# Performance work log

Hardware: AMD Instinct MI355X
Metric: run time of the kernel (lower is better)

The kernel has to match this reference:

```python
import jax, jax.numpy as jnp
import numpy as np

NUM_HEADS = 8
NUM_GROUPS = 8
EPS = 1e-5


def group_norm(x, gamma, beta):
    # x: [B, C, H, W], 8 groups over channel dim
    B, C, H, W = x.shape
    xg = x.reshape(B, NUM_GROUPS, C // NUM_GROUPS, H, W)
    mean = xg.mean(axis=(2, 3, 4), keepdims=True)
    var = xg.var(axis=(2, 3, 4), keepdims=True)
    xn = ((xg - mean) * jax.lax.rsqrt(var + EPS)).reshape(B, C, H, W)
    return xn * gamma[None, :, None, None] + beta[None, :, None, None]


def conv1x1(x, w, b):
    # w: [O, C] (1x1 conv kernel squeezed), x: [B, C, H, W]
    return jnp.einsum('oc,bchw->bohw', w, x) + b[None, :, None, None]


def setup_inputs() -> dict:
    key = jax.random.key(0)
    ks = jax.random.split(key, 6)
    B, C, H, W = 16, 512, 32, 32
    x = jax.random.normal(ks[0], (B, C, H, W), dtype=jnp.float32)
    norm_w = jnp.ones((C,), jnp.float32)
    norm_b = jnp.zeros((C,), jnp.float32)
    s = 1.0 / np.sqrt(C)
    qkv_w = jax.random.uniform(ks[1], (3 * C, C), jnp.float32, -s, s)
    qkv_b = jax.random.uniform(ks[2], (3 * C,), jnp.float32, -s, s)
    proj_w = jax.random.uniform(ks[3], (C, C), jnp.float32, -s, s)
    proj_b = jax.random.uniform(ks[4], (C,), jnp.float32, -s, s)
    return {"x": x, "norm_w": norm_w, "norm_b": norm_b,
            "qkv_w": qkv_w, "qkv_b": qkv_b, "proj_w": proj_w, "proj_b": proj_b}


def reference(x, norm_w, norm_b, qkv_w, qkv_b, proj_w, proj_b):
    B, C, H, W = x.shape
    hd = C // NUM_HEADS  # head dim
    h = group_norm(x, norm_w, norm_b)
    qkv = conv1x1(h, qkv_w, qkv_b)                 # [B, 3C, H, W]
    q, k, v = jnp.split(qkv, 3, axis=1)
    q = q.reshape(B, NUM_HEADS, hd, H * W)
    k = k.reshape(B, NUM_HEADS, hd, H * W)
    v = v.reshape(B, NUM_HEADS, hd, H * W)
    scale = hd ** (-0.5)
    attn = jax.nn.softmax(jnp.einsum('bhci,bhcj->bhij', q, k) * scale, axis=-1)
    h = jnp.einsum('bhij,bhcj->bhci', attn, v).reshape(B, C, H, W)
    h = conv1x1(h, proj_w, proj_b)
    return x + h
```

## Files before the change

### kernel.cpp

```cpp
#include <hip/hip_runtime.h>
#include <hip/hip_bf16.h>


typedef __bf16 bf16;
typedef __attribute__((ext_vector_type(8))) __bf16 bf16x8;
typedef __attribute__((ext_vector_type(4))) float f32x4;
typedef __attribute__((ext_vector_type(16))) float f32x16;
typedef __attribute__((ext_vector_type(4))) unsigned int u32x4;

#define SCALE_Q 0.18033688f

__device__ __forceinline__ bf16x8 ld8(const bf16* p) {
    return *reinterpret_cast<const bf16x8*>(p);
}

__device__ __forceinline__ void gl_lds16(const void* g, void* l) {
    __builtin_amdgcn_global_load_lds(
        (const __attribute__((address_space(1))) void*)g,
        (__attribute__((address_space(3))) void*)l, 16, 0, 0);
}

__global__ __launch_bounds__(256) void cvt_weights(const float* __restrict__ qkv_w,
                                                   const float* __restrict__ proj_w,
                                                   bf16* __restrict__ dst) {
    const int N1 = 1536 * 512;
    int i = (blockIdx.x * 256 + threadIdx.x) * 4;
    float4 f = (i < N1) ? *reinterpret_cast<const float4*>(qkv_w + i)
                        : *reinterpret_cast<const float4*>(proj_w + (i - N1));
    dst[i + 0] = (bf16)f.x;
    dst[i + 1] = (bf16)f.y;
    dst[i + 2] = (bf16)f.z;
    dst[i + 3] = (bf16)f.w;
}

__global__ __launch_bounds__(256) void gn_fused(const float* __restrict__ x,
                                                const float* __restrict__ gamma,
                                                const float* __restrict__ beta,
                                                bf16* __restrict__ hnT) {
    int bg = blockIdx.x;
    int b = bg >> 3, g = bg & 7;
    const float* base = x + (size_t)bg * 65536;
    int t = threadIdx.x;
    int wave = t >> 6, lane = t & 63;

    float s = 0.f, sq = 0.f;
    for (int i = t * 4; i < 65536; i += 256 * 4) {
        float4 f = *reinterpret_cast<const float4*>(base + i);
        s += f.x + f.y + f.z + f.w;
        sq += f.x * f.x + f.y * f.y + f.z * f.z + f.w * f.w;
    }
    #pragma unroll
    for (int off = 32; off > 0; off >>= 1) {
        s += __shfl_down(s, off);
        sq += __shfl_down(sq, off);
    }
    __shared__ float ls[4], lq[4];
    __shared__ float2 st;
    if (lane == 0) { ls[wave] = s; lq[wave] = sq; }
    __syncthreads();
    if (t == 0) {
        s = ls[0] + ls[1] + ls[2] + ls[3];
        sq = lq[0] + lq[1] + lq[2] + lq[3];
        float mean = s * (1.f / 65536.f);
        float var = sq * (1.f / 65536.f) - mean * mean;
        st = make_float2(mean, rsqrtf(var + 1e-5f));
    }
    __syncthreads();
    float mean = st.x, rstd = st.y;

    __shared__ float tile[64][65];
    int cl = t & 63;
    float ga = gamma[g * 64 + cl] * rstd;
    float be = beta[g * 64 + cl] - mean * ga;
    for (int pt = 0; pt < 16; pt++) {
        const float* xb = base + pt * 64;
        #pragma unroll
        for (int r = 0; r < 16; r++) {
            int crow = r * 4 + (t >> 6);
            tile[crow][t & 63] = xb[(size_t)crow * 1024 + (t & 63)];
        }
        __syncthreads();
        bf16* ob = hnT + ((size_t)b * 1024 + pt * 64) * 512 + g * 64 + cl;
        #pragma unroll
        for (int r = 0; r < 16; r++) {
            int pl = r * 4 + (t >> 6);
            ob[(size_t)pl * 512] = (bf16)(tile[cl][pl] * ga + be);
        }
        __syncthreads();
    }
}

__device__ __forceinline__ void gemm_stage(const bf16* __restrict__ A,
                                           const bf16* __restrict__ B,
                                           char* smem, int buf,
                                           int m_blk, int n_blk, int k0,
                                           int wave, int lane) {
    char* Al = smem + buf * 32768;
    char* Bl = Al + 16384;
    #pragma unroll
    for (int i = 0; i < 4; i++) {
        int seg = i * 4 + wave;
        int r = seg * 8 + (lane >> 3);
        int cg = (lane & 7) ^ (r & 7);
        gl_lds16((const char*)(A + (size_t)(m_blk + r) * 512 + k0) + cg * 16,
                 Al + seg * 1024);
        gl_lds16((const char*)(B + (size_t)(n_blk + r) * 512 + k0) + cg * 16,
                 Bl + seg * 1024);
    }
}

__device__ __forceinline__ void gemm_compute(const char* smem, int buf,
                                             int wave, int lane,
                                             f32x4 (&acc)[4][4]) {
    const char* Al = smem + buf * 32768;
    const char* Bl = Al + 16384;
    int l15 = lane & 15, hi = lane >> 4;
    int mb = (wave >> 1) * 64, nb = (wave & 1) * 64;
    #pragma unroll
    for (int kc = 0; kc < 2; kc++) {
        int ck = kc * 4 + hi;
        bf16x8 a[4], b[4];
        #pragma unroll
        for (int mf = 0; mf < 4; mf++) {
            int row = mb + mf * 16 + l15;
            a[mf] = *reinterpret_cast<const bf16x8*>(Al + row * 128 + (ck ^ (row & 7)) * 16);
        }
        #pragma unroll
        for (int nf = 0; nf < 4; nf++) {
            int row = nb + nf * 16 + l15;
            b[nf] = *reinterpret_cast<const bf16x8*>(Bl + row * 128 + (ck ^ (row & 7)) * 16);
        }
        #pragma unroll
        for (int mf = 0; mf < 4; mf++)
            #pragma unroll
            for (int nf = 0; nf < 4; nf++)
                acc[mf][nf] = __builtin_amdgcn_mfma_f32_16x16x32_bf16(
                    a[mf], b[nf], acc[mf][nf], 0, 0, 0);
    }
}

#define GEMM_LDS_LOOP(A_, B_, SMEM_)                            \
    f32x4 acc[4][4] = {};                                       \
    {                                                           \
        gemm_stage(A_, B_, SMEM_, 0, m_blk, n_blk, 0, wave, lane); \
        __syncthreads();                                        \
        int buf = 0;                                            \
        for (int ks = 0; ks < 8; ks++) {                        \
            if (ks < 7)                                         \
                gemm_stage(A_, B_, SMEM_, buf ^ 1, m_blk, n_blk, (ks + 1) * 64, wave, lane); \
            gemm_compute(SMEM_, buf, wave, lane, acc);          \
            __syncthreads();                                    \
            buf ^= 1;                                           \
        }                                                       \
    }

__global__ __launch_bounds__(256, 2) void gemm_qkv(const bf16* __restrict__ hnT,
                                                   const bf16* __restrict__ wqkv,
                                                   const float* __restrict__ qkv_b,
                                                   bf16* __restrict__ qk_t,
                                                   bf16* __restrict__ vbuf) {
    __shared__ char smem[65536];
    int b = blockIdx.z;
    int wave = threadIdx.x >> 6, lane = threadIdx.x & 63;
    int l15 = lane & 15;
    int y = blockIdx.y;
    if (y < 8) {
        int m_blk = blockIdx.x * 128;
        int n_blk = y * 128;
        const bf16* A = hnT + (size_t)b * 1024 * 512;
        GEMM_LDS_LOOP(A, wqkv, smem)
        bf16* out = qk_t + (size_t)b * 1024 * 1024;
        int col0 = n_blk + (wave & 1) * 64 + l15;
        int row0 = m_blk + (wave >> 1) * 64 + (lane >> 4) * 4;
        #pragma unroll
        for (int nf = 0; nf < 4; nf++) {
            int col = col0 + nf * 16;
            float bias = qkv_b[col];
            float scl = (col < 512) ? SCALE_Q : 1.0f;
            #pragma unroll
            for (int mf = 0; mf < 4; mf++)
                #pragma unroll
                for (int r = 0; r < 4; r++)
                    out[(size_t)(row0 + mf * 16 + r) * 1024 + col] =
                        (bf16)((acc[mf][nf][r] + bias) * scl);
        }
    } else {
        int m_blk = (y - 8) * 128;
        int n_blk = blockIdx.x * 128;
        const bf16* A = wqkv + (size_t)1024 * 512;
        const bf16* Bm = hnT + (size_t)b * 1024 * 512;
        GEMM_LDS_LOOP(A, Bm, smem)
        bf16* out = vbuf + (size_t)b * 512 * 1024;
        int col0 = n_blk + (wave & 1) * 64 + l15;
        int row0 = m_blk + (wave >> 1) * 64 + (lane >> 4) * 4;
        #pragma unroll
        for (int mf = 0; mf < 4; mf++)
            #pragma unroll
            for (int r = 0; r < 4; r++) {
                int row = row0 + mf * 16 + r;
                float bias = qkv_b[1024 + row];
                #pragma unroll
                for (int nf = 0; nf < 4; nf++)
                    out[(size_t)row * 1024 + col0 + nf * 16] = (bf16)(acc[mf][nf][r] + bias);
            }
    }
}

__global__ __launch_bounds__(256, 2) void gemm_proj(const bf16* __restrict__ wproj,
                                                    const bf16* __restrict__ attnT,
                                                    const float* __restrict__ proj_b,
                                                    const float* __restrict__ x,
                                                    float* __restrict__ out) {
    __shared__ char smem[65536];
    int b = blockIdx.z;
    int wave = threadIdx.x >> 6, lane = threadIdx.x & 63;
    int m_blk = blockIdx.x * 128;
    int n_blk = blockIdx.y * 128;
    const bf16* Bm = attnT + (size_t)b * 1024 * 512;
    GEMM_LDS_LOOP(wproj, Bm, smem)
    const float* xb = x + (size_t)b * 512 * 1024;
    float* ob = out + (size_t)b * 512 * 1024;
    int l15 = lane & 15;
    int col0 = n_blk + (wave & 1) * 64 + l15;
    int row0 = m_blk + (wave >> 1) * 64 + (lane >> 4) * 4;
    #pragma unroll
    for (int mf = 0; mf < 4; mf++)
        #pragma unroll
        for (int r = 0; r < 4; r++) {
            int row = row0 + mf * 16 + r;
            float bias = proj_b[row];
            #pragma unroll
            for (int nf = 0; nf < 4; nf++) {
                size_t idx = (size_t)row * 1024 + col0 + nf * 16;
                ob[idx] = acc[mf][nf][r] + bias + xb[idx];
            }
        }
}

__global__ __launch_bounds__(256, 4) void attn_kernel(const bf16* __restrict__ qk_t,
                                                      const bf16* __restrict__ vbuf,
                                                      bf16* __restrict__ attnT) {
    int flat = blockIdx.x;
    int it = flat >> 7;
    int bh = flat & 127;
    int b = bh >> 3, h = bh & 7;
    int wave = threadIdx.x >> 6, lane = threadIdx.x & 63;
    int l31 = lane & 31, hi = lane >> 5;
    int i0 = it * 128 + wave * 32;
    const bf16* qkb = qk_t + (size_t)b * 1024 * 1024;
    const bf16* kbase = qkb + 512 + h * 64;
    const bf16* vb = vbuf + ((size_t)b * 512 + h * 64) * 1024;

    __shared__ __align__(16) char smem[32768];

    bf16x8 bq[4];
    #pragma unroll
    for (int kc = 0; kc < 4; kc++)
        bq[kc] = ld8(qkb + (size_t)(i0 + l31) * 1024 + h * 64 + kc * 16 + hi * 8);

    f32x16 oacc[2] = {};
    float l_part = 0.f;

#define ATTN_STAGE(bufi, j0_)                                                        \
    {                                                                                \
        char* Kl = smem + (bufi) * 16384;                                            \
        char* Vl = Kl + 8192;                                                        \
        _Pragma("unroll")                                                            \
        for (int i = 0; i < 2; i++) {                                                \
            int seg = wave + i * 4;                                                  \
            int r = seg * 8 + (lane >> 3);                                           \
            int cg = (lane & 7) ^ (r & 7);                                           \
            gl_lds16((const char*)(kbase + (size_t)((j0_) + r) * 1024) + cg * 16,    \
                     Kl + seg * 1024);                                               \
            gl_lds16((const char*)(vb + (size_t)r * 1024 + (j0_)) + cg * 16,         \
                     Vl + seg * 1024);                                               \
        }                                                                            \
    }

    ATTN_STAGE(0, 0)
    int buf = 0;

    for (int t = 0; t < 16; t++) {
        asm volatile("" ::: "memory");
        __builtin_amdgcn_s_barrier();
        if (t < 15) {
            ATTN_STAGE(buf ^ 1, (t + 1) * 64)
            asm volatile("s_waitcnt vmcnt(4)" ::: "memory");
        } else {
            asm volatile("s_waitcnt vmcnt(0)" ::: "memory");
        }
        __builtin_amdgcn_s_barrier();
        asm volatile("" ::: "memory");

        const char* Kl = smem + buf * 16384;
        const char* Vl = Kl + 8192;
        int rx = l31 & 7;

        bf16x8 kf[2][4];
        #pragma unroll
        for (int jb = 0; jb < 2; jb++)
            #pragma unroll
            for (int kc = 0; kc < 4; kc++)
                kf[jb][kc] = *reinterpret_cast<const bf16x8*>(
                    Kl + (jb * 32 + l31) * 128 + ((kc * 2 + hi) ^ rx) * 16);

        f32x16 s[2] = {};
        #pragma unroll
        for (int kc = 0; kc < 4; kc++) {
            s[0] = __builtin_amdgcn_mfma_f32_32x32x16_bf16(kf[0][kc], bq[kc], s[0], 0, 0, 0);
            s[1] = __builtin_amdgcn_mfma_f32_32x32x16_bf16(kf[1][kc], bq[kc], s[1], 0, 0, 0);
        }

        bf16x8 vf[2][4];
        #pragma unroll
        for (int df = 0; df < 2; df++)
            #pragma unroll
            for (int ks = 0; ks < 4; ks++)
                vf[df][ks] = *reinterpret_cast<const bf16x8*>(
                    Vl + (df * 32 + l31) * 128 + ((ks * 2 + hi) ^ rx) * 16);

        unsigned int pk0[2][4], pk1[2][4];
        #pragma unroll
        for (int jb = 0; jb < 2; jb++)
            #pragma unroll
            for (int m = 0; m < 4; m++) {
                float e0 = exp2f(s[jb][m * 4 + 0]);
                float e1 = exp2f(s[jb][m * 4 + 1]);
                float e2 = exp2f(s[jb][m * 4 + 2]);
                float e3 = exp2f(s[jb][m * 4 + 3]);
                l_part += (e0 + e1) + (e2 + e3);
                asm("v_cvt_pk_bf16_f32 %0, %1, %2" : "=v"(pk0[jb][m]) : "v"(e0), "v"(e1));
                asm("v_cvt_pk_bf16_f32 %0, %1, %2" : "=v"(pk1[jb][m]) : "v"(e2), "v"(e3));
            }

        bf16x8 af[4];
        #pragma unroll
        for (int jb = 0; jb < 2; jb++)
            #pragma unroll
            for (int tt = 0; tt < 2; tt++) {
                unsigned int a0 = pk0[jb][tt * 2], b0 = pk0[jb][tt * 2 + 1];
                unsigned int a1 = pk1[jb][tt * 2], b1 = pk1[jb][tt * 2 + 1];
                asm("v_permlane32_swap_b32 %0, %1" : "+v"(a0), "+v"(b0));
                asm("v_permlane32_swap_b32 %0, %1" : "+v"(a1), "+v"(b1));
                u32x4 w = {a0, a1, b0, b1};
                af[jb * 2 + tt] = __builtin_bit_cast(bf16x8, w);
            }

        #pragma unroll
        for (int ks = 0; ks < 4; ks++) {
            oacc[0] = __builtin_amdgcn_mfma_f32_32x32x16_bf16(af[ks], vf[0][ks], oacc[0], 0, 0, 0);
            oacc[1] = __builtin_amdgcn_mfma_f32_32x32x16_bf16(af[ks], vf[1][ks], oacc[1], 0, 0, 0);
        }

        buf ^= 1;
    }
#undef ATTN_STAGE

    float lsum = l_part + __shfl_xor(l_part, 32);
    float inv = 1.f / lsum;

    __syncthreads();

    bf16* O_l = (bf16*)smem;
    #pragma unroll
    for (int reg = 0; reg < 16; reg++) {
        int qrow = (reg & 3) + 8 * (reg >> 2) + 4 * hi;
        float iv = __shfl(inv, qrow);
        O_l[(wave * 32 + qrow) * 72 + l31]      = (bf16)(oacc[0][reg] * iv);
        O_l[(wave * 32 + qrow) * 72 + 32 + l31] = (bf16)(oacc[1][reg] * iv);
    }
    __syncthreads();
    {
        int tt = threadIdx.x;
        int il = tt >> 1, half = tt & 1;
        const bf16* lsrc = O_l + il * 72 + half * 32;
        bf16* gdst = attnT + ((size_t)b * 1024 + it * 128 + il) * 512 + h * 64 + half * 32;
        #pragma unroll
        for (int k = 0; k < 4; k++)
            *reinterpret_cast<bf16x8*>(gdst + k * 8) =
                *reinterpret_cast<const bf16x8*>(lsrc + k * 8);
    }
}

extern "C" void kernel_launch(void* const* d_in, const int* in_sizes, int n_in,
                              void* d_out, int out_size, void* d_ws, size_t ws_size,
                              hipStream_t stream) {
    (void)in_sizes; (void)n_in; (void)out_size; (void)ws_size;
    const float* x      = (const float*)d_in[0];
    const float* norm_w = (const float*)d_in[1];
    const float* norm_b = (const float*)d_in[2];
    const float* qkv_w  = (const float*)d_in[3];
    const float* qkv_b  = (const float*)d_in[4];
    const float* proj_w = (const float*)d_in[5];
    const float* proj_b = (const float*)d_in[6];
    float* out = (float*)d_out;

    char* w = (char*)d_ws;
    bf16* wqkv  = (bf16*)w;
    bf16* wproj = wqkv + (size_t)1536 * 512;
    bf16* hnT   = wproj + (size_t)512 * 512;
    bf16* qk_t  = hnT + (size_t)16 * 1024 * 512;
    bf16* vbuf  = qk_t + (size_t)16 * 1024 * 1024;
    bf16* attnT = vbuf + (size_t)16 * 512 * 1024;

    cvt_weights<<<1024, 256, 0, stream>>>(qkv_w, proj_w, wqkv);
    gn_fused<<<128, 256, 0, stream>>>(x, norm_w, norm_b, hnT);
    gemm_qkv<<<dim3(8, 12, 16), 256, 0, stream>>>(hnT, wqkv, qkv_b, qk_t, vbuf);
    attn_kernel<<<1024, 256, 0, stream>>>(qk_t, vbuf, attnT);
    gemm_proj<<<dim3(4, 8, 16), 256, 0, stream>>>(wproj, attnT, proj_b, x, out);
}
```

Before: 147.6 us.

## Merge weight-convert and groupnorm launches; unroll attention loop with static buffers

```diff
diff --git a/kernel.cpp b/kernel.cpp
--- a/kernel.cpp
+++ b/kernel.cpp
@@ -20,27 +20,31 @@
         (__attribute__((address_space(3))) void*)l, 16, 0, 0);
 }
 
-__global__ __launch_bounds__(256) void cvt_weights(const float* __restrict__ qkv_w,
-                                                   const float* __restrict__ proj_w,
-                                                   bf16* __restrict__ dst) {
-    const int N1 = 1536 * 512;
-    int i = (blockIdx.x * 256 + threadIdx.x) * 4;
-    float4 f = (i < N1) ? *reinterpret_cast<const float4*>(qkv_w + i)
-                        : *reinterpret_cast<const float4*>(proj_w + (i - N1));
-    dst[i + 0] = (bf16)f.x;
-    dst[i + 1] = (bf16)f.y;
-    dst[i + 2] = (bf16)f.z;
-    dst[i + 3] = (bf16)f.w;
-}
-
-__global__ __launch_bounds__(256) void gn_fused(const float* __restrict__ x,
-                                                const float* __restrict__ gamma,
-                                                const float* __restrict__ beta,
-                                                bf16* __restrict__ hnT) {
-    int bg = blockIdx.x;
+__global__ __launch_bounds__(256) void cvt_gn(const float* __restrict__ qkv_w,
+                                              const float* __restrict__ proj_w,
+                                              bf16* __restrict__ wdst,
+                                              const float* __restrict__ x,
+                                              const float* __restrict__ gamma,
+                                              const float* __restrict__ beta,
+                                              bf16* __restrict__ hnT) {
+    __shared__ float tile[64][65];
+    __shared__ float ls[4], lq[4];
+    __shared__ float2 st;
+    int t = threadIdx.x;
+    if (blockIdx.x < 1024) {
+        const int N1 = 1536 * 512;
+        int i = (blockIdx.x * 256 + t) * 4;
+        float4 f = (i < N1) ? *reinterpret_cast<const float4*>(qkv_w + i)
+                            : *reinterpret_cast<const float4*>(proj_w + (i - N1));
+        wdst[i + 0] = (bf16)f.x;
+        wdst[i + 1] = (bf16)f.y;
+        wdst[i + 2] = (bf16)f.z;
+        wdst[i + 3] = (bf16)f.w;
+        return;
+    }
+    int bg = blockIdx.x - 1024;
     int b = bg >> 3, g = bg & 7;
     const float* base = x + (size_t)bg * 65536;
-    int t = threadIdx.x;
     int wave = t >> 6, lane = t & 63;
 
     float s = 0.f, sq = 0.f;
@@ -54,8 +58,6 @@
         s += __shfl_down(s, off);
         sq += __shfl_down(sq, off);
     }
-    __shared__ float ls[4], lq[4];
-    __shared__ float2 st;
     if (lane == 0) { ls[wave] = s; lq[wave] = sq; }
     __syncthreads();
     if (t == 0) {
@@ -68,7 +70,6 @@
     __syncthreads();
     float mean = st.x, rstd = st.y;
 
-    __shared__ float tile[64][65];
     int cl = t & 63;
     float ga = gamma[g * 64 + cl] * rstd;
     float be = beta[g * 64 + cl] - mean * ga;
@@ -259,103 +260,111 @@
         bq[kc] = ld8(qkb + (size_t)(i0 + l31) * 1024 + h * 64 + kc * 16 + hi * 8);
 
     f32x16 oacc[2] = {};
-    float l_part = 0.f;
-
-#define ATTN_STAGE(bufi, j0_)                                                        \
-    {                                                                                \
-        char* Kl = smem + (bufi) * 16384;                                            \
-        char* Vl = Kl + 8192;                                                        \
-        _Pragma("unroll")                                                            \
-        for (int i = 0; i < 2; i++) {                                                \
-            int seg = wave + i * 4;                                                  \
-            int r = seg * 8 + (lane >> 3);                                           \
-            int cg = (lane & 7) ^ (r & 7);                                           \
-            gl_lds16((const char*)(kbase + (size_t)((j0_) + r) * 1024) + cg * 16,    \
-                     Kl + seg * 1024);                                               \
-            gl_lds16((const char*)(vb + (size_t)r * 1024 + (j0_)) + cg * 16,         \
-                     Vl + seg * 1024);                                               \
-        }                                                                            \
-    }
-
-    ATTN_STAGE(0, 0)
-    int buf = 0;
-
-    for (int t = 0; t < 16; t++) {
+    f32x4 l4 = {};
+
+    int srow = wave * 8 + (lane >> 3);
+    int cg = (lane & 7) ^ (lane >> 3);
+    const char* kp = (const char*)kbase + (size_t)srow * 2048 + cg * 16;
+    const char* vp = (const char*)vb + (size_t)srow * 2048 + cg * 16;
+    char* ldsK = smem + wave * 1024;
+
+#define ATTN_STAGE(BUFI)                                     \
+    {                                                        \
+        gl_lds16(kp,         ldsK + (BUFI) * 16384);         \
+        gl_lds16(kp + 65536, ldsK + (BUFI) * 16384 + 4096);  \
+        gl_lds16(vp,         ldsK + (BUFI) * 16384 + 8192);  \
+        gl_lds16(vp + 65536, ldsK + (BUFI) * 16384 + 12288); \
+        kp += 131072;                                        \
+        vp += 128;                                           \
+    }
+
+    int rx = l31 & 7;
+    int vaddr[4];
+    #pragma unroll
+    for (int k = 0; k < 4; k++) vaddr[k] = l31 * 128 + (((k * 2 + hi) ^ rx) * 16);
+
+#define ATTN_COMPUTE(BUFC)                                                              \
+    {                                                                                   \
+        bf16x8 kf[2][4];                                                                \
+        _Pragma("unroll")                                                               \
+        for (int jb = 0; jb < 2; jb++)                                                  \
+            _Pragma("unroll")                                                           \
+            for (int kc = 0; kc < 4; kc++)                                              \
+                kf[jb][kc] = *reinterpret_cast<const bf16x8*>(                          \
+                    smem + (BUFC) * 16384 + jb * 4096 + vaddr[kc]);                     \
+        f32x16 s[2] = {};                                                               \
+        _Pragma("unroll")                                                               \
+        for (int kc = 0; kc < 4; kc++) {                                                \
+            s[0] = __builtin_amdgcn_mfma_f32_32x32x16_bf16(kf[0][kc], bq[kc], s[0], 0, 0, 0); \
+            s[1] = __builtin_amdgcn_mfma_f32_32x32x16_bf16(kf[1][kc], bq[kc], s[1], 0, 0, 0); \
+        }                                                                               \
+        bf16x8 vf[2][4];                                                                \
+        _Pragma("unroll")                                                               \
+        for (int df = 0; df < 2; df++)                                                  \
+            _Pragma("unroll")                                                           \
+            for (int ks = 0; ks < 4; ks++)                                              \
+                vf[df][ks] = *reinterpret_cast<const bf16x8*>(                          \
+                    smem + (BUFC) * 16384 + 8192 + df * 4096 + vaddr[ks]);              \
+        unsigned int pk0[2][4], pk1[2][4];                                              \
+        _Pragma("unroll")                                                               \
+        for (int jb = 0; jb < 2; jb++)                                                  \
+            _Pragma("unroll")                                                           \
+            for (int m = 0; m < 4; m++) {                                               \
+                float e0 = exp2f(s[jb][m * 4 + 0]);                                     \
+                float e1 = exp2f(s[jb][m * 4 + 1]);                                     \
+                float e2 = exp2f(s[jb][m * 4 + 2]);                                     \
+                float e3 = exp2f(s[jb][m * 4 + 3]);                                     \
+                f32x4 ev = {e0, e1, e2, e3};                                            \
+                l4 += ev;                                                               \
+                asm("v_cvt_pk_bf16_f32 %0, %1, %2" : "=v"(pk0[jb][m]) : "v"(e0), "v"(e1)); \
+                asm("v_cvt_pk_bf16_f32 %0, %1, %2" : "=v"(pk1[jb][m]) : "v"(e2), "v"(e3)); \
+            }                                                                           \
+        bf16x8 af[4];                                                                   \
+        _Pragma("unroll")                                                               \
+        for (int jb = 0; jb < 2; jb++)                                                  \
+            _Pragma("unroll")                                                           \
+            for (int tt = 0; tt < 2; tt++) {                                            \
+                unsigned int a0 = pk0[jb][tt * 2], b0 = pk0[jb][tt * 2 + 1];            \
+                unsigned int a1 = pk1[jb][tt * 2], b1 = pk1[jb][tt * 2 + 1];            \
+                asm("v_permlane32_swap_b32 %0, %1" : "+v"(a0), "+v"(b0));               \
+                asm("v_permlane32_swap_b32 %0, %1" : "+v"(a1), "+v"(b1));               \
+                u32x4 w = {a0, a1, b0, b1};                                             \
+                af[jb * 2 + tt] = __builtin_bit_cast(bf16x8, w);                        \
+            }                                                                           \
+        _Pragma("unroll")                                                               \
+        for (int ks = 0; ks < 4; ks++) {                                                \
+            oacc[0] = __builtin_amdgcn_mfma_f32_32x32x16_bf16(af[ks], vf[0][ks], oacc[0], 0, 0, 0); \
+            oacc[1] = __builtin_amdgcn_mfma_f32_32x32x16_bf16(af[ks], vf[1][ks], oacc[1], 0, 0, 0); \
+        }                                                                               \
+    }
+
+    ATTN_STAGE(0)
+
+    for (int t = 0; t < 16; t += 2) {
         asm volatile("" ::: "memory");
         __builtin_amdgcn_s_barrier();
-        if (t < 15) {
-            ATTN_STAGE(buf ^ 1, (t + 1) * 64)
+        ATTN_STAGE(1)
+        asm volatile("s_waitcnt vmcnt(4)" ::: "memory");
+        __builtin_amdgcn_s_barrier();
+        asm volatile("" ::: "memory");
+        ATTN_COMPUTE(0)
+
+        asm volatile("" ::: "memory");
+        __builtin_amdgcn_s_barrier();
+        if (t < 14) {
+            ATTN_STAGE(0)
             asm volatile("s_waitcnt vmcnt(4)" ::: "memory");
         } else {
             asm volatile("s_waitcnt vmcnt(0)" ::: "memory");
         }
         __builtin_amdgcn_s_barrier();
         asm volatile("" ::: "memory");
-
-        const char* Kl = smem + buf * 16384;
-        const char* Vl = Kl + 8192;
-        int rx = l31 & 7;
-
-        bf16x8 kf[2][4];
-        #pragma unroll
-        for (int jb = 0; jb < 2; jb++)
-            #pragma unroll
-            for (int kc = 0; kc < 4; kc++)
-                kf[jb][kc] = *reinterpret_cast<const bf16x8*>(
-                    Kl + (jb * 32 + l31) * 128 + ((kc * 2 + hi) ^ rx) * 16);
-
-        f32x16 s[2] = {};
-        #pragma unroll
-        for (int kc = 0; kc < 4; kc++) {
-            s[0] = __builtin_amdgcn_mfma_f32_32x32x16_bf16(kf[0][kc], bq[kc], s[0], 0, 0, 0);
-            s[1] = __builtin_amdgcn_mfma_f32_32x32x16_bf16(kf[1][kc], bq[kc], s[1], 0, 0, 0);
-        }
-
-        bf16x8 vf[2][4];
-        #pragma unroll
-        for (int df = 0; df < 2; df++)
-            #pragma unroll
-            for (int ks = 0; ks < 4; ks++)
-                vf[df][ks] = *reinterpret_cast<const bf16x8*>(
-                    Vl + (df * 32 + l31) * 128 + ((ks * 2 + hi) ^ rx) * 16);
-
-        unsigned int pk0[2][4], pk1[2][4];
-        #pragma unroll
-        for (int jb = 0; jb < 2; jb++)
-            #pragma unroll
-            for (int m = 0; m < 4; m++) {
-                float e0 = exp2f(s[jb][m * 4 + 0]);
-                float e1 = exp2f(s[jb][m * 4 + 1]);
-                float e2 = exp2f(s[jb][m * 4 + 2]);
-                float e3 = exp2f(s[jb][m * 4 + 3]);
-                l_part += (e0 + e1) + (e2 + e3);
-                asm("v_cvt_pk_bf16_f32 %0, %1, %2" : "=v"(pk0[jb][m]) : "v"(e0), "v"(e1));
-                asm("v_cvt_pk_bf16_f32 %0, %1, %2" : "=v"(pk1[jb][m]) : "v"(e2), "v"(e3));
-            }
-
-        bf16x8 af[4];
-        #pragma unroll
-        for (int jb = 0; jb < 2; jb++)
-            #pragma unroll
-            for (int tt = 0; tt < 2; tt++) {
-                unsigned int a0 = pk0[jb][tt * 2], b0 = pk0[jb][tt * 2 + 1];
-                unsigned int a1 = pk1[jb][tt * 2], b1 = pk1[jb][tt * 2 + 1];
-                asm("v_permlane32_swap_b32 %0, %1" : "+v"(a0), "+v"(b0));
-                asm("v_permlane32_swap_b32 %0, %1" : "+v"(a1), "+v"(b1));
-                u32x4 w = {a0, a1, b0, b1};
-                af[jb * 2 + tt] = __builtin_bit_cast(bf16x8, w);
-            }
-
-        #pragma unroll
-        for (int ks = 0; ks < 4; ks++) {
-            oacc[0] = __builtin_amdgcn_mfma_f32_32x32x16_bf16(af[ks], vf[0][ks], oacc[0], 0, 0, 0);
-            oacc[1] = __builtin_amdgcn_mfma_f32_32x32x16_bf16(af[ks], vf[1][ks], oacc[1], 0, 0, 0);
-        }
-
-        buf ^= 1;
+        ATTN_COMPUTE(1)
     }
 #undef ATTN_STAGE
-
+#undef ATTN_COMPUTE
+
+    float l_part = (l4[0] + l4[1]) + (l4[2] + l4[3]);
     float lsum = l_part + __shfl_xor(l_part, 32);
     float inv = 1.f / lsum;
 
@@ -403,8 +412,7 @@
     bf16* vbuf  = qk_t + (size_t)16 * 1024 * 1024;
     bf16* attnT = vbuf + (size_t)16 * 512 * 1024;
 
-    cvt_weights<<<1024, 256, 0, stream>>>(qkv_w, proj_w, wqkv);
-    gn_fused<<<128, 256, 0, stream>>>(x, norm_w, norm_b, hnT);
+    cvt_gn<<<1152, 256, 0, stream>>>(qkv_w, proj_w, wqkv, x, norm_w, norm_b, hnT);
     gemm_qkv<<<dim3(8, 12, 16), 256, 0, stream>>>(hnT, wqkv, qkv_b, qk_t, vbuf);
     attn_kernel<<<1024, 256, 0, stream>>>(qk_t, vbuf, attnT);
     gemm_proj<<<dim3(4, 8, 16), 256, 0, stream>>>(wproj, attnT, proj_b, x, out);
```

New measurement: 160.8 us. 1.09x slower.
